# Performance work log

Measured on AMD Instinct MI355X. Metric: run time of the kernel, lower is better.

Reference implementation:

```python
import jax, jax.numpy as jnp
import numpy as np

N_EXPERTS = 256
N_GROUP = 8
TOPK_GROUP = 4
TOP_K = 8
ROUTED_SCALING = 2.5
HIDDEN = 7168


def setup_inputs() -> dict:
    key = jax.random.key(0)
    k1, k2, k3 = jax.random.split(key, 3)
    hidden_states = jax.random.normal(k1, (4, 4096, HIDDEN), dtype=jnp.float32)
    # kaiming_uniform(a=sqrt(5)) on [E, H] -> bound = 1/sqrt(H)
    bound = 1.0 / np.sqrt(HIDDEN)
    weight = jax.random.uniform(k2, (N_EXPERTS, HIDDEN), dtype=jnp.float32,
                                minval=-bound, maxval=bound)
    # buffer inits to zeros in torch; use small random values to exercise the bias path
    e_score_correction_bias = 0.01 * jax.random.normal(k3, (N_EXPERTS,), dtype=jnp.float32)
    return {"hidden_states": hidden_states, "weight": weight,
            "e_score_correction_bias": e_score_correction_bias}


def reference(hidden_states, weight, e_score_correction_bias):
    B, S, H = hidden_states.shape
    T = B * S
    x = hidden_states.reshape(T, H).astype(jnp.float32)
    # router logits: [T, E]
    logits = jnp.einsum('th,eh->te', x, weight)
    scores = jax.nn.sigmoid(logits)
    scores_for_choice = scores + e_score_correction_bias[None, :]
    # group score = sum of top-2 bias-adjusted scores within each group
    grp = scores_for_choice.reshape(T, N_GROUP, N_EXPERTS // N_GROUP)
    top2, _ = jax.lax.top_k(grp, 2)                      # [T, G, 2]
    group_scores = top2.sum(axis=-1)                     # [T, G]
    _, group_idx = jax.lax.top_k(group_scores, TOPK_GROUP)  # [T, topk_group]
    group_mask = jnp.zeros((T, N_GROUP), dtype=jnp.bool_)
    group_mask = group_mask.at[jnp.arange(T)[:, None], group_idx].set(True)
    score_mask = jnp.repeat(group_mask, N_EXPERTS // N_GROUP, axis=1)  # [T, E]
    masked_scores = jnp.where(score_mask, scores_for_choice, 0.0)
    _, topk_indices = jax.lax.top_k(masked_scores, TOP_K)  # [T, top_k]
    topk_weights = jnp.take_along_axis(scores, topk_indices, axis=1)
    denom = topk_weights.sum(axis=-1, keepdims=True) + 1e-20
    topk_weights = topk_weights / denom * ROUTED_SCALING
    return topk_indices, topk_weights
```

## Files before the change

### kernel.cpp

```cpp
#include <hip/hip_runtime.h>
#include <math.h>


#define HH 7168
#define EE 256
#define BMT 32
#define BK 32
#define NTH 256

typedef float v4f __attribute__((ext_vector_type(4)));

struct SMem {
    union {
        float wbuf[2][EE * BK];
        float logits[BMT][EE];
    } u;
    float xbuf[2][BMT * BK];
    float bias[EE];
};

__device__ __forceinline__ void gl16(const void* g, void* l) {
    __builtin_amdgcn_global_load_lds(
        (__attribute__((address_space(1))) const void*)g,
        (__attribute__((address_space(3))) void*)l, 16, 0, 0);
}

__global__ __launch_bounds__(NTH, 2)
void moe_gate(const float* __restrict__ x, const float* __restrict__ w,
              const float* __restrict__ bias, float* __restrict__ out, int T) {
    __shared__ SMem sm;
    const int tid = threadIdx.x;
    const int bm = blockIdx.x * BMT;
    sm.bias[tid] = bias[tid];
    const int lane = tid & 63;
    const int wv = __builtin_amdgcn_readfirstlane(tid >> 6);
    const int l3 = lane >> 3, l7 = lane & 7;

    const int cch = l7 ^ l3;
    const float* wsrc = w + (size_t)(wv * 64 + l3) * HH + cch * 4;
    const float* xsrc = x + (size_t)(bm + wv * 8 + l3) * HH + l7 * 4;
    float* const wdst0 = &sm.u.wbuf[0][wv * 64 * BK];
    float* const wdst1 = &sm.u.wbuf[1][wv * 64 * BK];
    float* const xdst0 = &sm.xbuf[0][wv * 8 * BK];
    float* const xdst1 = &sm.xbuf[1][wv * 8 * BK];

    float acc[8][4];
    #pragma unroll
    for (int t = 0; t < 8; ++t)
        #pragma unroll
        for (int j = 0; j < 4; ++j) acc[t][j] = 0.f;

    #pragma unroll
    for (int p = 0; p < 8; ++p)
        gl16(wsrc + (size_t)p * 8 * HH, wdst0 + p * 8 * BK);
    gl16(xsrc, xdst0);
    __syncthreads();

    const int NT = HH / BK;
    for (int ts = 0; ts < NT; ++ts) {
        const int b = ts & 1;
        if (ts + 1 < NT) {
            const int k1 = (ts + 1) * BK;
            float* wd = (b ? wdst0 : wdst1);
            float* xd = (b ? xdst0 : xdst1);
            #pragma unroll
            for (int p = 0; p < 8; ++p)
                gl16(wsrc + (size_t)p * 8 * HH + k1, wd + p * 8 * BK);
            gl16(xsrc + k1, xd);
        }
        const float* wl = sm.u.wbuf[b];
        const float* xl = &sm.xbuf[b][wv * 8 * BK];
        #pragma unroll
        for (int q = 0; q < 8; ++q) {
            const int wq = ((q ^ l7) << 2);
            v4f w0 = *(const v4f*)&wl[(lane      ) * BK + wq];
            v4f w1 = *(const v4f*)&wl[(lane +  64) * BK + wq];
            v4f w2 = *(const v4f*)&wl[(lane + 128) * BK + wq];
            v4f w3 = *(const v4f*)&wl[(lane + 192) * BK + wq];
            v4f xv[8];
            #pragma unroll
            for (int t = 0; t < 8; ++t)
                xv[t] = *(const v4f*)&xl[t * BK + q * 4];
            #pragma unroll
            for (int t = 0; t < 8; ++t) {
                #pragma unroll
                for (int c = 0; c < 4; ++c) {
                    float xs = xv[t][c];
                    acc[t][0] = fmaf(xs, w0[c], acc[t][0]);
                    acc[t][1] = fmaf(xs, w1[c], acc[t][1]);
                    acc[t][2] = fmaf(xs, w2[c], acc[t][2]);
                    acc[t][3] = fmaf(xs, w3[c], acc[t][3]);
                }
            }
        }
        __syncthreads();
    }

    #pragma unroll
    for (int t = 0; t < 8; ++t)
        #pragma unroll
        for (int j = 0; j < 4; ++j)
            sm.u.logits[wv * 8 + t][lane + 64 * j] = acc[t][j];
    __syncthreads();

    for (int tt = wv; tt < BMT; tt += 4) {
        const int gt = bm + tt;
        float4 lg = *(const float4*)&sm.u.logits[tt][lane * 4];
        float lgv[4] = {lg.x, lg.y, lg.z, lg.w};
        float s[4], sc[4], m[4];
        #pragma unroll
        for (int j = 0; j < 4; ++j) {
            float e = (float)exp(-(double)lgv[j]);
            float u = __fadd_rn(1.0f, e);
            s[j] = __fdiv_rn(1.0f, u);
            sc[j] = __fadd_rn(s[j], sm.bias[lane * 4 + j]);
        }
        float a1 = fmaxf(sc[0], sc[1]), a2 = fminf(sc[0], sc[1]);
        if (sc[2] > a1) { a2 = a1; a1 = sc[2]; } else a2 = fmaxf(a2, sc[2]);
        if (sc[3] > a1) { a2 = a1; a1 = sc[3]; } else a2 = fmaxf(a2, sc[3]);
        #pragma unroll
        for (int off = 1; off <= 4; off <<= 1) {
            float b1 = __shfl_xor(a1, off);
            float b2 = __shfl_xor(a2, off);
            float m1 = fmaxf(a1, b1);
            float m2 = fmaxf(fminf(a1, b1), (a1 >= b1) ? a2 : b2);
            a1 = m1; a2 = m2;
        }
        float gsc = __fadd_rn(a1, a2);
        float gsv[8];
        #pragma unroll
        for (int g = 0; g < 8; ++g) gsv[g] = __shfl(gsc, g * 8);
        int gm = lane >> 3;
        int rank = 0;
        #pragma unroll
        for (int hh = 0; hh < 8; ++hh)
            rank += (gsv[hh] > gsv[gm]) || (gsv[hh] == gsv[gm] && hh > gm);
        bool selg = rank < 4;
        #pragma unroll
        for (int j = 0; j < 4; ++j) m[j] = selg ? sc[j] : 0.0f;

        float selw = 0.f; int seli = 0;
        #pragma unroll
        for (int k = 0; k < 8; ++k) {
            float bv = m[0]; int bj = 0;
            #pragma unroll
            for (int j = 1; j < 4; ++j)
                if (m[j] >= bv) { bv = m[j]; bj = j; }
            float v = bv; int ii = lane * 4 + bj;
            #pragma unroll
            for (int off = 1; off < 64; off <<= 1) {
                float ov = __shfl_xor(v, off);
                int oi = __shfl_xor(ii, off);
                if (ov > v || (ov == v && oi > ii)) { v = ov; ii = oi; }
            }
            int oj = ii & 3, ol = ii >> 2;
            float cand = (oj == 0) ? s[0] : (oj == 1) ? s[1]
                       : (oj == 2) ? s[2] : s[3];
            float wgt = __shfl(cand, ol);
            if (lane == k) { seli = ii; selw = wgt; }
            if (lane == ol) {
                if (oj == 0) m[0] = -1e30f;
                else if (oj == 1) m[1] = -1e30f;
                else if (oj == 2) m[2] = -1e30f;
                else m[3] = -1e30f;
            }
        }
        float wk[8];
        #pragma unroll
        for (int k = 0; k < 8; ++k) wk[k] = __shfl(selw, k);
        float denom = __fadd_rn(
            __fadd_rn(__fadd_rn(wk[0], wk[1]), __fadd_rn(wk[2], wk[3])),
            __fadd_rn(__fadd_rn(wk[4], wk[5]), __fadd_rn(wk[6], wk[7])));
        denom = __fadd_rn(denom, 1e-20f);
        if (lane < 8) {
            out[(size_t)gt * 8 + lane] = (float)seli;
            out[(size_t)T * 8 + (size_t)gt * 8 + lane] =
                __fmul_rn(__fdiv_rn(selw, denom), 2.5f);
        }
    }
}

extern "C" void kernel_launch(void* const* d_in, const int* in_sizes, int n_in,
                              void* d_out, int out_size, void* d_ws, size_t ws_size,
                              hipStream_t stream) {
    const float* x    = (const float*)d_in[0];
    const float* w    = (const float*)d_in[1];
    const float* bias = (const float*)d_in[2];
    float* out = (float*)d_out;
    const int T = in_sizes[0] / HH;
    moe_gate<<<T / BMT, NTH, 0, stream>>>(x, w, bias, out, T);
}
```

Before: 882.9 us.

## Halve block to two waves with 16 tokens per wave and software-pipelined LDS reads

The block shrinks from 4 waves to 2, and each wave now computes 16 tokens × 256 experts instead of 8, doubling register accumulators. Each thread now issues twice as many global-to-LDS weight and x loads. The inner k-loop double-buffers LDS reads into registers so the next slice's weight and x vectors load while the current slice's FMAs run. The aim is more FMAs per LDS read of weights, at the cost of higher register pressure and fewer waves to hide latency (launch bounds now 1).

New measurement: 1.073 ms. 21.6% more time.

```diff
diff --git a/kernel.cpp b/kernel.cpp
--- a/kernel.cpp
+++ b/kernel.cpp
@@ -6,7 +6,9 @@
 #define EE 256
 #define BMT 32
 #define BK 32
-#define NTH 256
+#define NTH 128
+#define TW 16
+#define NT (HH / BK)
 
 typedef float v4f __attribute__((ext_vector_type(4)));
 
@@ -25,85 +27,97 @@
         (__attribute__((address_space(3))) void*)l, 16, 0, 0);
 }
 
-__global__ __launch_bounds__(NTH, 2)
+#define LOADW(dst, wl, q) do { const int wq_ = (((q) ^ l7) << 2);            \
+    dst[0] = *(const v4f*)&(wl)[(lane      ) * BK + wq_];                    \
+    dst[1] = *(const v4f*)&(wl)[(lane +  64) * BK + wq_];                    \
+    dst[2] = *(const v4f*)&(wl)[(lane + 128) * BK + wq_];                    \
+    dst[3] = *(const v4f*)&(wl)[(lane + 192) * BK + wq_]; } while (0)
+
+#define LOADX(dst, xl, q) do { _Pragma("unroll")                             \
+    for (int t_ = 0; t_ < TW; ++t_)                                          \
+        dst[t_] = *(const v4f*)&(xl)[t_ * BK + (q) * 4]; } while (0)
+
+#define FMAB(xr, wr) do { _Pragma("unroll")                                  \
+    for (int t_ = 0; t_ < TW; ++t_) { _Pragma("unroll")                      \
+        for (int c_ = 0; c_ < 4; ++c_) {                                     \
+            const float xs_ = xr[t_][c_];                                    \
+            acc[t_][0] = fmaf(xs_, wr[0][c_], acc[t_][0]);                   \
+            acc[t_][1] = fmaf(xs_, wr[1][c_], acc[t_][1]);                   \
+            acc[t_][2] = fmaf(xs_, wr[2][c_], acc[t_][2]);                   \
+            acc[t_][3] = fmaf(xs_, wr[3][c_], acc[t_][3]); } } } while (0)
+
+__global__ __launch_bounds__(NTH, 1)
 void moe_gate(const float* __restrict__ x, const float* __restrict__ w,
               const float* __restrict__ bias, float* __restrict__ out, int T) {
     __shared__ SMem sm;
     const int tid = threadIdx.x;
     const int bm = blockIdx.x * BMT;
     sm.bias[tid] = bias[tid];
+    sm.bias[tid + 128] = bias[tid + 128];
     const int lane = tid & 63;
     const int wv = __builtin_amdgcn_readfirstlane(tid >> 6);
-    const int l3 = lane >> 3, l7 = lane & 7;
-
-    const int cch = l7 ^ l3;
-    const float* wsrc = w + (size_t)(wv * 64 + l3) * HH + cch * 4;
-    const float* xsrc = x + (size_t)(bm + wv * 8 + l3) * HH + l7 * 4;
-    float* const wdst0 = &sm.u.wbuf[0][wv * 64 * BK];
-    float* const wdst1 = &sm.u.wbuf[1][wv * 64 * BK];
-    float* const xdst0 = &sm.xbuf[0][wv * 8 * BK];
-    float* const xdst1 = &sm.xbuf[1][wv * 8 * BK];
-
-    float acc[8][4];
+    const int l3 = (lane >> 3) & 7, l7 = lane & 7;
+
+    const float* wsrc = w + (size_t)(wv * 128 + l3) * HH + ((l7 ^ l3) << 2);
+    float* const wdst0 = &sm.u.wbuf[0][wv * 128 * BK];
+    float* const wdst1 = &sm.u.wbuf[1][wv * 128 * BK];
+
+    const int tok0 = tid >> 3;
+    const float* xsrc0 = x + (size_t)(bm + tok0) * HH + (l7 << 2);
+    const float* xsrc1 = xsrc0 + (size_t)16 * HH;
+    float* const xd00 = &sm.xbuf[0][wv * 256];
+    float* const xd01 = &sm.xbuf[0][wv * 256 + 512];
+    float* const xd10 = &sm.xbuf[1][wv * 256];
+    float* const xd11 = &sm.xbuf[1][wv * 256 + 512];
+
+    float acc[TW][4];
     #pragma unroll
-    for (int t = 0; t < 8; ++t)
+    for (int t = 0; t < TW; ++t)
         #pragma unroll
         for (int j = 0; j < 4; ++j) acc[t][j] = 0.f;
 
     #pragma unroll
-    for (int p = 0; p < 8; ++p)
+    for (int p = 0; p < 16; ++p)
         gl16(wsrc + (size_t)p * 8 * HH, wdst0 + p * 8 * BK);
-    gl16(xsrc, xdst0);
+    gl16(xsrc0, xd00);
+    gl16(xsrc1, xd01);
     __syncthreads();
 
-    const int NT = HH / BK;
     for (int ts = 0; ts < NT; ++ts) {
         const int b = ts & 1;
         if (ts + 1 < NT) {
             const int k1 = (ts + 1) * BK;
-            float* wd = (b ? wdst0 : wdst1);
-            float* xd = (b ? xdst0 : xdst1);
+            float* wd = b ? wdst0 : wdst1;
             #pragma unroll
-            for (int p = 0; p < 8; ++p)
+            for (int p = 0; p < 16; ++p)
                 gl16(wsrc + (size_t)p * 8 * HH + k1, wd + p * 8 * BK);
-            gl16(xsrc + k1, xd);
-        }
-        const float* wl = sm.u.wbuf[b];
-        const float* xl = &sm.xbuf[b][wv * 8 * BK];
-        #pragma unroll
-        for (int q = 0; q < 8; ++q) {
-            const int wq = ((q ^ l7) << 2);
-            v4f w0 = *(const v4f*)&wl[(lane      ) * BK + wq];
-            v4f w1 = *(const v4f*)&wl[(lane +  64) * BK + wq];
-            v4f w2 = *(const v4f*)&wl[(lane + 128) * BK + wq];
-            v4f w3 = *(const v4f*)&wl[(lane + 192) * BK + wq];
-            v4f xv[8];
-            #pragma unroll
-            for (int t = 0; t < 8; ++t)
-                xv[t] = *(const v4f*)&xl[t * BK + q * 4];
-            #pragma unroll
-            for (int t = 0; t < 8; ++t) {
-                #pragma unroll
-                for (int c = 0; c < 4; ++c) {
-                    float xs = xv[t][c];
-                    acc[t][0] = fmaf(xs, w0[c], acc[t][0]);
-                    acc[t][1] = fmaf(xs, w1[c], acc[t][1]);
-                    acc[t][2] = fmaf(xs, w2[c], acc[t][2]);
-                    acc[t][3] = fmaf(xs, w3[c], acc[t][3]);
-                }
-            }
-        }
+            gl16(xsrc0 + k1, b ? xd00 : xd10);
+            gl16(xsrc1 + k1, b ? xd01 : xd11);
+        }
+        const float* wl = b ? sm.u.wbuf[1] : sm.u.wbuf[0];
+        const float* xl = (b ? &sm.xbuf[1][0] : &sm.xbuf[0][0]) + wv * 512;
+
+        v4f wA[4], wB[4], xA[TW], xB[TW];
+        LOADW(wA, wl, 0); LOADX(xA, xl, 0);
+        LOADW(wB, wl, 1); LOADX(xB, xl, 1); FMAB(xA, wA);
+        LOADW(wA, wl, 2); LOADX(xA, xl, 2); FMAB(xB, wB);
+        LOADW(wB, wl, 3); LOADX(xB, xl, 3); FMAB(xA, wA);
+        LOADW(wA, wl, 4); LOADX(xA, xl, 4); FMAB(xB, wB);
+        LOADW(wB, wl, 5); LOADX(xB, xl, 5); FMAB(xA, wA);
+        LOADW(wA, wl, 6); LOADX(xA, xl, 6); FMAB(xB, wB);
+        LOADW(wB, wl, 7); LOADX(xB, xl, 7); FMAB(xA, wA);
+        FMAB(xB, wB);
         __syncthreads();
     }
 
     #pragma unroll
-    for (int t = 0; t < 8; ++t)
+    for (int t = 0; t < TW; ++t)
         #pragma unroll
         for (int j = 0; j < 4; ++j)
-            sm.u.logits[wv * 8 + t][lane + 64 * j] = acc[t][j];
+            sm.u.logits[wv * TW + t][lane + 64 * j] = acc[t][j];
     __syncthreads();
 
-    for (int tt = wv; tt < BMT; tt += 4) {
+    for (int tt = wv; tt < BMT; tt += 2) {
         const int gt = bm + tt;
         float4 lg = *(const float4*)&sm.u.logits[tt][lane * 4];
         float lgv[4] = {lg.x, lg.y, lg.z, lg.w};
```
